# Kernel optimization log

Measured on AMD Instinct MI355X. Metric: run time of the kernel, lower is better.

The kernel has to match this reference:

```python
import jax, jax.numpy as jnp
import numpy as np

STEP_SIZE = 0.01  # init kwarg step_size

def _quad_grad(A, b, x):
    # grad of per-node quadratic: 2*A_n @ x_n + b_n ; shapes [N,D,D],[N,D],[N,D]
    return 2.0 * jnp.einsum('nij,nj->ni', A, x) + b

def setup_inputs() -> dict:
    key = jax.random.key(0)
    kA, kb, kx, ke = jax.random.split(key, 4)
    N, D, E = 20000, 64, 320000
    A = jax.random.normal(kA, (N, D, D), dtype=jnp.float32)
    b = jax.random.normal(kb, (N, D), dtype=jnp.float32)
    x = jax.random.normal(kx, (N, D), dtype=jnp.float32)
    edge_index = jax.random.randint(ke, (2, E), 0, N, dtype=jnp.int64)
    return {"A": A, "b": b, "x": x, "edge_index": edge_index, "num_layers": 10}

def reference(A, b, x, edge_index, num_layers):
    N, D = x.shape
    src, dst = edge_index[0], edge_index[1]
    # push-sum column-stochastic mixing weights: 1/out_degree incl. self-loop
    deg = jnp.ones((N,), x.dtype).at[src].add(1.0)
    inv_deg = (1.0 / deg)[:, None]  # [N,1]

    def mix(z):  # z: [N,F]
        msg = z[src] * inv_deg[src]  # gather + weight
        agg = jax.ops.segment_sum(msg, dst, num_segments=N)
        return agg + z * inv_deg  # self-loop term

    y = _quad_grad(A, b, x)
    u = x
    v = jnp.ones((N, 1), x.dtype)
    x0 = x
    x1 = x0
    for _ in range(num_layers):
        u = mix(u - STEP_SIZE * y)          # conv on u
        v = mix(v)                           # conv on v (push-sum weight)
        x1 = u * (1.0 / v)                   # inv_v * u
        g1 = _quad_grad(A, b, x1)
        g0 = _quad_grad(A, b, x0)
        y = mix(y) + g1 - g0                 # conv on y + gradient tracking
        x0 = x1
    comm_cost = jnp.asarray(3 * num_layers * src.shape[0], dtype=jnp.int64)
    return x1, comm_cost
```

## Files before the change

kernel.cpp:

```cpp
#include <hip/hip_runtime.h>
#include <hip/hip_bf16.h>
#include <hip/hip_fp16.h>

#define STEP 0.01f
#define D 64
#define NUM_LAYERS 10

union H4 { uint2 u; __half h[4]; };
union H8 { uint4 u; __half2 h2[4]; __half h[8]; };


__global__ void k_setup(float* __restrict__ degf, int* __restrict__ degd, int N) {
    int n = blockIdx.x * blockDim.x + threadIdx.x;
    if (n < N) { degf[n] = 1.0f; degd[n] = 0; }
}

__global__ void k_deg2(const int* __restrict__ ei, float* __restrict__ degf,
                       int* __restrict__ degd, int E) {
    int e = blockIdx.x * blockDim.x + threadIdx.x;
    if (e < E) {
        unsafeAtomicAdd(&degf[ei[e]], 1.0f);
        atomicAdd(&degd[ei[E + e]], 1);
    }
}

__global__ __launch_bounds__(1024) void k_scan(
        const int* __restrict__ degd, const float* __restrict__ degf,
        int* __restrict__ row_ptr, int* __restrict__ cursor,
        float* __restrict__ invdeg, int N, int E) {
    __shared__ int part[1024];
    int tid = threadIdx.x;
    int chunk = (N + 1023) / 1024;
    int lo = tid * chunk, hi = min(lo + chunk, N);
    int s = 0;
    for (int i = lo; i < hi; ++i) s += degd[i];
    part[tid] = s;
    __syncthreads();
    for (int off = 1; off < 1024; off <<= 1) {
        int v = (tid >= off) ? part[tid - off] : 0;
        __syncthreads();
        part[tid] += v;
        __syncthreads();
    }
    int base = (tid == 0) ? 0 : part[tid - 1];
    for (int i = lo; i < hi; ++i) {
        row_ptr[i] = base;
        cursor[i] = base;
        base += degd[i];
        invdeg[i] = 1.0f / degf[i];
    }
    if (tid == 1023) row_ptr[N] = E;
}

__global__ void k_scatter(const int* __restrict__ ei, int* __restrict__ cursor,
                          int* __restrict__ col, int E) {
    int e = blockIdx.x * blockDim.x + threadIdx.x;
    if (e < E) {
        int pos = atomicAdd(&cursor[ei[E + e]], 1);
        col[pos] = ei[e];
    }
}


__global__ __launch_bounds__(256) void k_init(
        const float* __restrict__ A, const float* __restrict__ b,
        const float* __restrict__ x, const float* __restrict__ invdeg,
        __half* __restrict__ Ah, __half2* __restrict__ msg,
        float* __restrict__ vw, float* __restrict__ x0, int N) {
    __shared__ __align__(16) float sx[D];
    __shared__ float syv[D];
    int n = blockIdx.x, t = threadIdx.x;
    int lane = t & 63, w = t >> 6, colgrp = lane & 15;
    if (t < D) sx[t] = x[(size_t)n * D + t];
    __syncthreads();
    const float* An = A + (size_t)n * D * D;
    __half* Ahn = Ah + (size_t)n * D * D;
    float4 xr = ((const float4*)sx)[colgrp];
    int rbase = w * 16 + (lane >> 4);
#pragma unroll
    for (int g = 0; g < 4; ++g) {
        int row = rbase + g * 4;
        float4 a = ((const float4*)(An + (size_t)row * D))[colgrp];
        H4 pk;
        pk.h[0] = __float2half(a.x);
        pk.h[1] = __float2half(a.y);
        pk.h[2] = __float2half(a.z);
        pk.h[3] = __float2half(a.w);
        ((uint2*)(Ahn + (size_t)row * D))[colgrp] = pk.u;
        float p = a.x * xr.x + a.y * xr.y + a.z * xr.z + a.w * xr.w;
        p += __shfl_xor(p, 1);
        p += __shfl_xor(p, 2);
        p += __shfl_xor(p, 4);
        p += __shfl_xor(p, 8);
        if (colgrp == 0) syv[row] = 2.0f * p + b[(size_t)n * D + row];
    }
    __syncthreads();
    if (t < D) {
        float wd = invdeg[n];
        float xv = sx[t];
        float yv = syv[t];
        msg[(size_t)n * D + t] = __floats2half2_rn((xv - STEP * yv) * wd, yv * wd);
        x0[(size_t)n * D + t] = xv;
        if (t == 0) vw[n] = wd;
    }
}


__global__ __launch_bounds__(256) void k_layer(
        const __half* __restrict__ Ah,
        const int* __restrict__ row_ptr, const int* __restrict__ col,
        const __half2* __restrict__ msg, const float* __restrict__ vw,
        const float* __restrict__ invdeg,
        __half2* __restrict__ msgn, float* __restrict__ vwn,
        float* __restrict__ x0, float* __restrict__ xout,
        int last_idx, float comm, int N) {
    int t = threadIdx.x;
    int lane = t & 63, w = t >> 6;
    int n = blockIdx.x * 4 + w;
    if (n >= N) return;

    int j = lane >> 4, q4 = lane & 15;
    int rs = row_ptr[n], re = row_ptr[n + 1];

    const uint4* Ap = (const uint4*)(Ah + (size_t)n * D * D);
    uint4 a[8];
#pragma unroll
    for (int k = 0; k < 8; ++k) a[k] = Ap[lane + 64 * k];

    size_t off = (size_t)n * D + lane;
    float2 msf = __half22float2(msg[off]);
    float x0v = x0[off];
    float vwn_self = vw[n];
    float invd = invdeg[n];

    float4 au = {0.f, 0.f, 0.f, 0.f}, ay = {0.f, 0.f, 0.f, 0.f};
    float av = 0.0f;
    for (int base = rs; base < re; base += 8) {
        int e0 = base + (j << 1), e1 = e0 + 1;
        bool b0 = e0 < re, b1 = e1 < re;
        int s0 = 0, s1 = 0;
        if (b0) s0 = col[e0];
        if (b1) s1 = col[e1];
        H8 m0, m1;
        m0.u = make_uint4(0u, 0u, 0u, 0u);
        m1.u = make_uint4(0u, 0u, 0u, 0u);
        float w0 = 0.f, w1 = 0.f;
        if (b0) m0.u = ((const uint4*)(msg + (size_t)s0 * D))[q4];
        if (b1) m1.u = ((const uint4*)(msg + (size_t)s1 * D))[q4];
        if (b0 && q4 == 0) w0 = vw[s0];
        if (b1 && q4 == 0) w1 = vw[s1];
        float2 f0 = __half22float2(m0.h2[0]);
        float2 f1 = __half22float2(m0.h2[1]);
        float2 f2 = __half22float2(m0.h2[2]);
        float2 f3 = __half22float2(m0.h2[3]);
        au.x += f0.x; ay.x += f0.y;
        au.y += f1.x; ay.y += f1.y;
        au.z += f2.x; ay.z += f2.y;
        au.w += f3.x; ay.w += f3.y;
        f0 = __half22float2(m1.h2[0]);
        f1 = __half22float2(m1.h2[1]);
        f2 = __half22float2(m1.h2[2]);
        f3 = __half22float2(m1.h2[3]);
        au.x += f0.x; ay.x += f0.y;
        au.y += f1.x; ay.y += f1.y;
        au.z += f2.x; ay.z += f2.y;
        au.w += f3.x; ay.w += f3.y;
        av += w0 + w1;
    }
    au.x += __shfl_xor(au.x, 16); au.y += __shfl_xor(au.y, 16);
    au.z += __shfl_xor(au.z, 16); au.w += __shfl_xor(au.w, 16);
    au.x += __shfl_xor(au.x, 32); au.y += __shfl_xor(au.y, 32);
    au.z += __shfl_xor(au.z, 32); au.w += __shfl_xor(au.w, 32);
    ay.x += __shfl_xor(ay.x, 16); ay.y += __shfl_xor(ay.y, 16);
    ay.z += __shfl_xor(ay.z, 16); ay.w += __shfl_xor(ay.w, 16);
    ay.x += __shfl_xor(ay.x, 32); ay.y += __shfl_xor(ay.y, 32);
    ay.z += __shfl_xor(ay.z, 32); ay.w += __shfl_xor(ay.w, 32);
    av += __shfl_xor(av, 16);
    av += __shfl_xor(av, 32);
    av = __shfl(av, 0);

    int src = lane >> 2, c = lane & 3;
    float ua = __shfl(au.x, src), ub = __shfl(au.y, src),
          uc = __shfl(au.z, src), ud = __shfl(au.w, src);
    float ya = __shfl(ay.x, src), yb = __shfl(ay.y, src),
          yc = __shfl(ay.z, src), yd = __shfl(ay.w, src);
    float ut = (c & 2) ? ((c & 1) ? ud : uc) : ((c & 1) ? ub : ua);
    float yt = (c & 2) ? ((c & 1) ? yd : yc) : ((c & 1) ? yb : ya);
    ut += msf.x;
    yt += msf.y;

    float vt = av + vwn_self;
    float rvt = __builtin_amdgcn_rcpf(vt);
    float x1 = ut * rvt;
    float dx = x1 - x0v;
    x0[off] = x1;
    if (xout) xout[off] = x1;
    if (lane == 0) vwn[n] = vt * invd;
    if (xout && n == 0 && lane == 0) xout[last_idx] = comm;

    int cb = (lane & 7) * 8;
    float dxv[8];
#pragma unroll
    for (int jj = 0; jj < 8; ++jj) dxv[jj] = __shfl(dx, cb + jj);

    float pk[8];
#pragma unroll
    for (int k = 0; k < 8; ++k) {
        H8 aa; aa.u = a[k];
        float p = 0.f;
#pragma unroll
        for (int jj = 0; jj < 8; ++jj)
            p += __half2float(aa.h[jj]) * dxv[jj];
        p += __shfl_xor(p, 1);
        p += __shfl_xor(p, 2);
        p += __shfl_xor(p, 4);
        pk[k] = p;
    }
    int srcg = (lane & 7) * 8;
    float pr[8];
#pragma unroll
    for (int k = 0; k < 8; ++k) pr[k] = __shfl(pk[k], srcg);
    int kk = lane >> 3;
    float prow = (kk & 4) ? ((kk & 2) ? ((kk & 1) ? pr[7] : pr[6])
                                      : ((kk & 1) ? pr[5] : pr[4]))
                          : ((kk & 2) ? ((kk & 1) ? pr[3] : pr[2])
                                      : ((kk & 1) ? pr[1] : pr[0]));
    float yn = yt + 2.0f * prow;
    msgn[off] = __floats2half2_rn((ut - STEP * yn) * invd, yn * invd);
}


extern "C" void kernel_launch(void* const* d_in, const int* in_sizes, int n_in,
                              void* d_out, int out_size, void* d_ws, size_t ws_size,
                              hipStream_t stream) {
    const float* A  = (const float*)d_in[0];
    const float* b  = (const float*)d_in[1];
    const float* x  = (const float*)d_in[2];
    const int*   ei = (const int*)d_in[3];

    const int N = in_sizes[1] / D;
    const int E = in_sizes[3] / 2;
    const size_t ND = (size_t)N * D;

    char* ws = (char*)d_ws;
    __half* Ah = (__half*)ws;
    __half2* msg0 = (__half2*)(ws + ND * D * sizeof(__half));
    __half2* msg1 = msg0 + ND;
    float* x0   = (float*)(msg1 + ND);
    float* vw0  = x0 + ND;
    float* vw1  = vw0 + N;
    float* invdeg = vw1 + N;
    float* degf = invdeg + N;
    int* degd    = (int*)(degf + N);
    int* row_ptr = degd + N;
    int* cursor  = row_ptr + N + 4;
    int* col     = cursor + N;

    k_setup<<<(N + 255) / 256, 256, 0, stream>>>(degf, degd, N);
    k_deg2<<<(E + 255) / 256, 256, 0, stream>>>(ei, degf, degd, E);
    k_scan<<<1, 1024, 0, stream>>>(degd, degf, row_ptr, cursor, invdeg, N, E);
    k_scatter<<<(E + 255) / 256, 256, 0, stream>>>(ei, cursor, col, E);
    k_init<<<N, 256, 0, stream>>>(A, b, x, invdeg, Ah, msg0, vw0, x0, N);

    float comm = (float)(3 * NUM_LAYERS * E);
    __half2 *mc = msg0, *mn = msg1;
    float *vc = vw0, *vn = vw1;
    for (int l = 0; l < NUM_LAYERS; ++l) {
        float* xout = (l == NUM_LAYERS - 1) ? (float*)d_out : nullptr;
        k_layer<<<(N + 3) / 4, 256, 0, stream>>>(Ah, row_ptr, col, mc, vc, invdeg,
                                                 mn, vn, x0, xout, out_size - 1, comm, N);
        __half2* tm = mc; mc = mn; mn = tm;
        float* tv = vc; vc = vn; vn = tv;
    }
}
```

Measured before the change: 960.6 us.

## Fuse init and all layers into one persistent cooperative kernel with grid syncs

Replaces the init kernel and ten per-layer launches with a single cooperative kernel of 1024 blocks. Each wave loops over nodes with a grid stride, and grid.sync separates the layers. The intent is to remove launch overhead and tail effects between layers. The cross-lane shuffle reductions are also replaced by per-wave shared-memory staging of dx and row results. The risk is grid-sync cost, lower occupancy from the fixed grid size, and bandwidth-bound layers that may gain little.

```diff
diff --git a/kernel.cpp b/kernel.cpp
--- a/kernel.cpp
+++ b/kernel.cpp
@@ -1,12 +1,14 @@
 #include <hip/hip_runtime.h>
-#include <hip/hip_bf16.h>
 #include <hip/hip_fp16.h>
+#include <hip/hip_cooperative_groups.h>
+
+namespace cg = cooperative_groups;
 
 #define STEP 0.01f
 #define D 64
 #define NUM_LAYERS 10
-
-union H4 { uint2 u; __half h[4]; };
+#define GRID 1024
+
 union H8 { uint4 u; __half2 h2[4]; __half h[8]; };
 
 
@@ -61,172 +63,179 @@
     }
 }
 
-
-__global__ __launch_bounds__(256) void k_init(
+__global__ void k_tail(float* __restrict__ out, int last_idx, int E) {
+    if (threadIdx.x == 0 && blockIdx.x == 0)
+        out[last_idx] = (float)(3 * NUM_LAYERS * E);
+}
+
+
+__global__ __launch_bounds__(256, 4) void k_fused(
         const float* __restrict__ A, const float* __restrict__ b,
-        const float* __restrict__ x, const float* __restrict__ invdeg,
-        __half* __restrict__ Ah, __half2* __restrict__ msg,
-        float* __restrict__ vw, float* __restrict__ x0, int N) {
-    __shared__ __align__(16) float sx[D];
-    __shared__ float syv[D];
-    int n = blockIdx.x, t = threadIdx.x;
-    int lane = t & 63, w = t >> 6, colgrp = lane & 15;
-    if (t < D) sx[t] = x[(size_t)n * D + t];
-    __syncthreads();
-    const float* An = A + (size_t)n * D * D;
-    __half* Ahn = Ah + (size_t)n * D * D;
-    float4 xr = ((const float4*)sx)[colgrp];
-    int rbase = w * 16 + (lane >> 4);
+        const float* __restrict__ x,
+        const int* __restrict__ row_ptr, const int* __restrict__ col,
+        const float* __restrict__ invdeg,
+        __half* __restrict__ Ah,
+        __half2* __restrict__ msg0, __half2* __restrict__ msg1,
+        float* __restrict__ vw0, float* __restrict__ vw1,
+        float* __restrict__ x0, float* __restrict__ xout,
+        int N) {
+    cg::grid_group gg = cg::this_grid();
+
+    __shared__ float sdx[4][D];
+    __shared__ float srow[4][D];
+    __shared__ float4 sg[4][2][16];
+
+    int t = threadIdx.x, lane = t & 63, w = t >> 6;
+    int wid = blockIdx.x * 4 + w;
+    int nw = GRID * 4;
+    int kq = lane >> 3;
+    int cb = (lane & 7) * 8;
+    int j = lane >> 4, q4 = lane & 15;
+
+    for (int n = wid; n < N; n += nw) {
+        size_t off = (size_t)n * D + lane;
+        float xv = x[off];
+        sdx[w][lane] = xv;
+        const float4* An = (const float4*)(A + (size_t)n * D * D);
+        uint4* Ahn = (uint4*)(Ah + (size_t)n * D * D);
 #pragma unroll
-    for (int g = 0; g < 4; ++g) {
-        int row = rbase + g * 4;
-        float4 a = ((const float4*)(An + (size_t)row * D))[colgrp];
-        H4 pk;
-        pk.h[0] = __float2half(a.x);
-        pk.h[1] = __float2half(a.y);
-        pk.h[2] = __float2half(a.z);
-        pk.h[3] = __float2half(a.w);
-        ((uint2*)(Ahn + (size_t)row * D))[colgrp] = pk.u;
-        float p = a.x * xr.x + a.y * xr.y + a.z * xr.z + a.w * xr.w;
-        p += __shfl_xor(p, 1);
-        p += __shfl_xor(p, 2);
-        p += __shfl_xor(p, 4);
-        p += __shfl_xor(p, 8);
-        if (colgrp == 0) syv[row] = 2.0f * p + b[(size_t)n * D + row];
-    }
-    __syncthreads();
-    if (t < D) {
+        for (int k = 0; k < 8; ++k) {
+            int row = kq + 8 * k;
+            int fidx = row * (D / 4) + (cb >> 2);
+            float4 f0 = An[fidx];
+            float4 f1 = An[fidx + 1];
+            H8 pk;
+            pk.h[0] = __float2half(f0.x);
+            pk.h[1] = __float2half(f0.y);
+            pk.h[2] = __float2half(f0.z);
+            pk.h[3] = __float2half(f0.w);
+            pk.h[4] = __float2half(f1.x);
+            pk.h[5] = __float2half(f1.y);
+            pk.h[6] = __float2half(f1.z);
+            pk.h[7] = __float2half(f1.w);
+            Ahn[lane + 64 * k] = pk.u;
+            float p = f0.x * sdx[w][cb + 0] + f0.y * sdx[w][cb + 1]
+                    + f0.z * sdx[w][cb + 2] + f0.w * sdx[w][cb + 3]
+                    + f1.x * sdx[w][cb + 4] + f1.y * sdx[w][cb + 5]
+                    + f1.z * sdx[w][cb + 6] + f1.w * sdx[w][cb + 7];
+            p += __shfl_xor(p, 1);
+            p += __shfl_xor(p, 2);
+            p += __shfl_xor(p, 4);
+            if ((lane & 7) == 0) srow[w][row] = p;
+        }
+        float yv = 2.0f * srow[w][lane] + b[off];
         float wd = invdeg[n];
-        float xv = sx[t];
-        float yv = syv[t];
-        msg[(size_t)n * D + t] = __floats2half2_rn((xv - STEP * yv) * wd, yv * wd);
-        x0[(size_t)n * D + t] = xv;
-        if (t == 0) vw[n] = wd;
-    }
-}
-
-
-__global__ __launch_bounds__(256) void k_layer(
-        const __half* __restrict__ Ah,
-        const int* __restrict__ row_ptr, const int* __restrict__ col,
-        const __half2* __restrict__ msg, const float* __restrict__ vw,
-        const float* __restrict__ invdeg,
-        __half2* __restrict__ msgn, float* __restrict__ vwn,
-        float* __restrict__ x0, float* __restrict__ xout,
-        int last_idx, float comm, int N) {
-    int t = threadIdx.x;
-    int lane = t & 63, w = t >> 6;
-    int n = blockIdx.x * 4 + w;
-    if (n >= N) return;
-
-    int j = lane >> 4, q4 = lane & 15;
-    int rs = row_ptr[n], re = row_ptr[n + 1];
-
-    const uint4* Ap = (const uint4*)(Ah + (size_t)n * D * D);
-    uint4 a[8];
+        msg0[off] = __floats2half2_rn((xv - STEP * yv) * wd, yv * wd);
+        x0[off] = xv;
+        if (lane == 0) vw0[n] = wd;
+    }
+    __threadfence();
+    gg.sync();
+
+    for (int l = 0; l < NUM_LAYERS; ++l) {
+        const __half2* mc = (l & 1) ? msg1 : msg0;
+        __half2* mn = (l & 1) ? msg0 : msg1;
+        const float* vc = (l & 1) ? vw1 : vw0;
+        float* vn = (l & 1) ? vw0 : vw1;
+        float* xo = (l == NUM_LAYERS - 1) ? xout : nullptr;
+
+        for (int n = wid; n < N; n += nw) {
+            int rs = row_ptr[n], re = row_ptr[n + 1];
+
+            const uint4* Ap = (const uint4*)(Ah + (size_t)n * D * D);
+            uint4 a[8];
 #pragma unroll
-    for (int k = 0; k < 8; ++k) a[k] = Ap[lane + 64 * k];
-
-    size_t off = (size_t)n * D + lane;
-    float2 msf = __half22float2(msg[off]);
-    float x0v = x0[off];
-    float vwn_self = vw[n];
-    float invd = invdeg[n];
-
-    float4 au = {0.f, 0.f, 0.f, 0.f}, ay = {0.f, 0.f, 0.f, 0.f};
-    float av = 0.0f;
-    for (int base = rs; base < re; base += 8) {
-        int e0 = base + (j << 1), e1 = e0 + 1;
-        bool b0 = e0 < re, b1 = e1 < re;
-        int s0 = 0, s1 = 0;
-        if (b0) s0 = col[e0];
-        if (b1) s1 = col[e1];
-        H8 m0, m1;
-        m0.u = make_uint4(0u, 0u, 0u, 0u);
-        m1.u = make_uint4(0u, 0u, 0u, 0u);
-        float w0 = 0.f, w1 = 0.f;
-        if (b0) m0.u = ((const uint4*)(msg + (size_t)s0 * D))[q4];
-        if (b1) m1.u = ((const uint4*)(msg + (size_t)s1 * D))[q4];
-        if (b0 && q4 == 0) w0 = vw[s0];
-        if (b1 && q4 == 0) w1 = vw[s1];
-        float2 f0 = __half22float2(m0.h2[0]);
-        float2 f1 = __half22float2(m0.h2[1]);
-        float2 f2 = __half22float2(m0.h2[2]);
-        float2 f3 = __half22float2(m0.h2[3]);
-        au.x += f0.x; ay.x += f0.y;
-        au.y += f1.x; ay.y += f1.y;
-        au.z += f2.x; ay.z += f2.y;
-        au.w += f3.x; ay.w += f3.y;
-        f0 = __half22float2(m1.h2[0]);
-        f1 = __half22float2(m1.h2[1]);
-        f2 = __half22float2(m1.h2[2]);
-        f3 = __half22float2(m1.h2[3]);
-        au.x += f0.x; ay.x += f0.y;
-        au.y += f1.x; ay.y += f1.y;
-        au.z += f2.x; ay.z += f2.y;
-        au.w += f3.x; ay.w += f3.y;
-        av += w0 + w1;
-    }
-    au.x += __shfl_xor(au.x, 16); au.y += __shfl_xor(au.y, 16);
-    au.z += __shfl_xor(au.z, 16); au.w += __shfl_xor(au.w, 16);
-    au.x += __shfl_xor(au.x, 32); au.y += __shfl_xor(au.y, 32);
-    au.z += __shfl_xor(au.z, 32); au.w += __shfl_xor(au.w, 32);
-    ay.x += __shfl_xor(ay.x, 16); ay.y += __shfl_xor(ay.y, 16);
-    ay.z += __shfl_xor(ay.z, 16); ay.w += __shfl_xor(ay.w, 16);
-    ay.x += __shfl_xor(ay.x, 32); ay.y += __shfl_xor(ay.y, 32);
-    ay.z += __shfl_xor(ay.z, 32); ay.w += __shfl_xor(ay.w, 32);
-    av += __shfl_xor(av, 16);
-    av += __shfl_xor(av, 32);
-    av = __shfl(av, 0);
-
-    int src = lane >> 2, c = lane & 3;
-    float ua = __shfl(au.x, src), ub = __shfl(au.y, src),
-          uc = __shfl(au.z, src), ud = __shfl(au.w, src);
-    float ya = __shfl(ay.x, src), yb = __shfl(ay.y, src),
-          yc = __shfl(ay.z, src), yd = __shfl(ay.w, src);
-    float ut = (c & 2) ? ((c & 1) ? ud : uc) : ((c & 1) ? ub : ua);
-    float yt = (c & 2) ? ((c & 1) ? yd : yc) : ((c & 1) ? yb : ya);
-    ut += msf.x;
-    yt += msf.y;
-
-    float vt = av + vwn_self;
-    float rvt = __builtin_amdgcn_rcpf(vt);
-    float x1 = ut * rvt;
-    float dx = x1 - x0v;
-    x0[off] = x1;
-    if (xout) xout[off] = x1;
-    if (lane == 0) vwn[n] = vt * invd;
-    if (xout && n == 0 && lane == 0) xout[last_idx] = comm;
-
-    int cb = (lane & 7) * 8;
-    float dxv[8];
+            for (int k = 0; k < 8; ++k) a[k] = Ap[lane + 64 * k];
+
+            size_t off = (size_t)n * D + lane;
+            float2 msf = __half22float2(mc[off]);
+            float x0v = x0[off];
+            float vws = vc[n];
+            float invd = invdeg[n];
+
+            float4 au = {0.f, 0.f, 0.f, 0.f}, ay = {0.f, 0.f, 0.f, 0.f};
+            float av = 0.0f;
+            for (int base = rs; base < re; base += 8) {
+                int e0 = base + (j << 1), e1 = e0 + 1;
+                bool b0 = e0 < re, b1 = e1 < re;
+                int s0 = 0, s1 = 0;
+                if (b0) s0 = col[e0];
+                if (b1) s1 = col[e1];
+                H8 m0, m1;
+                m0.u = make_uint4(0u, 0u, 0u, 0u);
+                m1.u = make_uint4(0u, 0u, 0u, 0u);
+                float w0 = 0.f, w1 = 0.f;
+                if (b0) m0.u = ((const uint4*)(mc + (size_t)s0 * D))[q4];
+                if (b1) m1.u = ((const uint4*)(mc + (size_t)s1 * D))[q4];
+                if (b0 && q4 == 0) w0 = vc[s0];
+                if (b1 && q4 == 0) w1 = vc[s1];
+                float2 f0 = __half22float2(m0.h2[0]);
+                float2 f1 = __half22float2(m0.h2[1]);
+                float2 f2 = __half22float2(m0.h2[2]);
+                float2 f3 = __half22float2(m0.h2[3]);
+                au.x += f0.x; ay.x += f0.y;
+                au.y += f1.x; ay.y += f1.y;
+                au.z += f2.x; ay.z += f2.y;
+                au.w += f3.x; ay.w += f3.y;
+                f0 = __half22float2(m1.h2[0]);
+                f1 = __half22float2(m1.h2[1]);
+                f2 = __half22float2(m1.h2[2]);
+                f3 = __half22float2(m1.h2[3]);
+                au.x += f0.x; ay.x += f0.y;
+                au.y += f1.x; ay.y += f1.y;
+                au.z += f2.x; ay.z += f2.y;
+                au.w += f3.x; ay.w += f3.y;
+                av += w0 + w1;
+            }
+            au.x += __shfl_xor(au.x, 16); au.y += __shfl_xor(au.y, 16);
+            au.z += __shfl_xor(au.z, 16); au.w += __shfl_xor(au.w, 16);
+            au.x += __shfl_xor(au.x, 32); au.y += __shfl_xor(au.y, 32);
+            au.z += __shfl_xor(au.z, 32); au.w += __shfl_xor(au.w, 32);
+            ay.x += __shfl_xor(ay.x, 16); ay.y += __shfl_xor(ay.y, 16);
+            ay.z += __shfl_xor(ay.z, 16); ay.w += __shfl_xor(ay.w, 16);
+            ay.x += __shfl_xor(ay.x, 32); ay.y += __shfl_xor(ay.y, 32);
+            ay.z += __shfl_xor(ay.z, 32); ay.w += __shfl_xor(ay.w, 32);
+            av += __shfl_xor(av, 16);
+            av += __shfl_xor(av, 32);
+            av = __shfl(av, 0);
+
+            if (j == 0) { sg[w][0][q4] = au; sg[w][1][q4] = ay; }
+            float ut = ((const float*)sg[w][0])[lane] + msf.x;
+            float yt = ((const float*)sg[w][1])[lane] + msf.y;
+
+            float vt = av + vws;
+            float rvt = __builtin_amdgcn_rcpf(vt);
+            float x1 = ut * rvt;
+            float dx = x1 - x0v;
+            x0[off] = x1;
+            if (xo) xo[off] = x1;
+            if (lane == 0) vn[n] = vt * invd;
+
+            sdx[w][lane] = dx;
 #pragma unroll
-    for (int jj = 0; jj < 8; ++jj) dxv[jj] = __shfl(dx, cb + jj);
-
-    float pk[8];
-#pragma unroll
-    for (int k = 0; k < 8; ++k) {
-        H8 aa; aa.u = a[k];
-        float p = 0.f;
-#pragma unroll
-        for (int jj = 0; jj < 8; ++jj)
-            p += __half2float(aa.h[jj]) * dxv[jj];
-        p += __shfl_xor(p, 1);
-        p += __shfl_xor(p, 2);
-        p += __shfl_xor(p, 4);
-        pk[k] = p;
-    }
-    int srcg = (lane & 7) * 8;
-    float pr[8];
-#pragma unroll
-    for (int k = 0; k < 8; ++k) pr[k] = __shfl(pk[k], srcg);
-    int kk = lane >> 3;
-    float prow = (kk & 4) ? ((kk & 2) ? ((kk & 1) ? pr[7] : pr[6])
-                                      : ((kk & 1) ? pr[5] : pr[4]))
-                          : ((kk & 2) ? ((kk & 1) ? pr[3] : pr[2])
-                                      : ((kk & 1) ? pr[1] : pr[0]));
-    float yn = yt + 2.0f * prow;
-    msgn[off] = __floats2half2_rn((ut - STEP * yn) * invd, yn * invd);
+            for (int k = 0; k < 8; ++k) {
+                H8 aa; aa.u = a[k];
+                float p = __half2float(aa.h[0]) * sdx[w][cb + 0]
+                        + __half2float(aa.h[1]) * sdx[w][cb + 1]
+                        + __half2float(aa.h[2]) * sdx[w][cb + 2]
+                        + __half2float(aa.h[3]) * sdx[w][cb + 3]
+                        + __half2float(aa.h[4]) * sdx[w][cb + 4]
+                        + __half2float(aa.h[5]) * sdx[w][cb + 5]
+                        + __half2float(aa.h[6]) * sdx[w][cb + 6]
+                        + __half2float(aa.h[7]) * sdx[w][cb + 7];
+                p += __shfl_xor(p, 1);
+                p += __shfl_xor(p, 2);
+                p += __shfl_xor(p, 4);
+                if ((lane & 7) == 0) srow[w][kq + 8 * k] = p;
+            }
+            float yn = yt + 2.0f * srow[w][lane];
+            mn[off] = __floats2half2_rn((ut - STEP * yn) * invd, yn * invd);
+        }
+        if (l != NUM_LAYERS - 1) {
+            __threadfence();
+            gg.sync();
+        }
+    }
 }
 
 
@@ -260,16 +269,19 @@
     k_deg2<<<(E + 255) / 256, 256, 0, stream>>>(ei, degf, degd, E);
     k_scan<<<1, 1024, 0, stream>>>(degd, degf, row_ptr, cursor, invdeg, N, E);
     k_scatter<<<(E + 255) / 256, 256, 0, stream>>>(ei, cursor, col, E);
-    k_init<<<N, 256, 0, stream>>>(A, b, x, invdeg, Ah, msg0, vw0, x0, N);
-
-    float comm = (float)(3 * NUM_LAYERS * E);
-    __half2 *mc = msg0, *mn = msg1;
-    float *vc = vw0, *vn = vw1;
-    for (int l = 0; l < NUM_LAYERS; ++l) {
-        float* xout = (l == NUM_LAYERS - 1) ? (float*)d_out : nullptr;
-        k_layer<<<(N + 3) / 4, 256, 0, stream>>>(Ah, row_ptr, col, mc, vc, invdeg,
-                                                 mn, vn, x0, xout, out_size - 1, comm, N);
-        __half2* tm = mc; mc = mn; mn = tm;
-        float* tv = vc; vc = vn; vn = tv;
-    }
-}
+
+    float* xout = (float*)d_out;
+    int Nv = N;
+
+    void* args[] = {
+        (void*)&A, (void*)&b, (void*)&x,
+        (void*)&row_ptr, (void*)&col, (void*)&invdeg,
+        (void*)&Ah, (void*)&msg0, (void*)&msg1,
+        (void*)&vw0, (void*)&vw1, (void*)&x0, (void*)&xout,
+        (void*)&Nv
+    };
+    hipLaunchCooperativeKernel((void*)k_fused, dim3(GRID), dim3(256),
+                               args, 0, stream);
+
+    k_tail<<<1, 64, 0, stream>>>(xout, out_size - 1, E);
+}
```

Measured after the change: 3.295 ms. +243.0%, slower.

## Split fused layer kernel into separate gather and matvec kernels

Applied to the files above, without the earlier changes.

Splits each layer into a neighbor-gather kernel, which writes dx, u and y to global scratch buffers, and a separate kernel that loads the fp16 A block and computes the matvec. Each kernel then holds fewer live registers, since the gather no longer keeps the 8 uint4 A fragments resident, and each should get higher occupancy. The cost is an extra round trip of three N*D float buffers through memory and double the number of launches per layer. The comm-cost write moves to a small tail kernel.

```diff
diff --git a/kernel.cpp b/kernel.cpp
--- a/kernel.cpp
+++ b/kernel.cpp
@@ -61,6 +61,11 @@
     }
 }
 
+__global__ void k_tail(float* __restrict__ out, int last_idx, int E) {
+    if (threadIdx.x == 0 && blockIdx.x == 0)
+        out[last_idx] = (float)(3 * NUM_LAYERS * E);
+}
+
 
 __global__ __launch_bounds__(256) void k_init(
         const float* __restrict__ A, const float* __restrict__ b,
@@ -106,14 +111,13 @@
 }
 
 
-__global__ __launch_bounds__(256) void k_layer(
-        const __half* __restrict__ Ah,
+__global__ __launch_bounds__(256) void k_gather(
         const int* __restrict__ row_ptr, const int* __restrict__ col,
         const __half2* __restrict__ msg, const float* __restrict__ vw,
         const float* __restrict__ invdeg,
-        __half2* __restrict__ msgn, float* __restrict__ vwn,
-        float* __restrict__ x0, float* __restrict__ xout,
-        int last_idx, float comm, int N) {
+        float* __restrict__ vwn, float* __restrict__ x0, float* __restrict__ xout,
+        float* __restrict__ dxb, float* __restrict__ utb, float* __restrict__ ytb,
+        int N) {
     int t = threadIdx.x;
     int lane = t & 63, w = t >> 6;
     int n = blockIdx.x * 4 + w;
@@ -121,17 +125,6 @@
 
     int j = lane >> 4, q4 = lane & 15;
     int rs = row_ptr[n], re = row_ptr[n + 1];
-
-    const uint4* Ap = (const uint4*)(Ah + (size_t)n * D * D);
-    uint4 a[8];
-#pragma unroll
-    for (int k = 0; k < 8; ++k) a[k] = Ap[lane + 64 * k];
-
-    size_t off = (size_t)n * D + lane;
-    float2 msf = __half22float2(msg[off]);
-    float x0v = x0[off];
-    float vwn_self = vw[n];
-    float invd = invdeg[n];
 
     float4 au = {0.f, 0.f, 0.f, 0.f}, ay = {0.f, 0.f, 0.f, 0.f};
     float av = 0.0f;
@@ -167,6 +160,13 @@
         au.w += f3.x; ay.w += f3.y;
         av += w0 + w1;
     }
+
+    size_t off = (size_t)n * D + lane;
+    float2 msf = __half22float2(msg[off]);
+    float x0v = x0[off];
+    float vws = vw[n];
+    float invd = invdeg[n];
+
     au.x += __shfl_xor(au.x, 16); au.y += __shfl_xor(au.y, 16);
     au.z += __shfl_xor(au.z, 16); au.w += __shfl_xor(au.w, 16);
     au.x += __shfl_xor(au.x, 32); au.y += __shfl_xor(au.y, 32);
@@ -189,19 +189,46 @@
     ut += msf.x;
     yt += msf.y;
 
-    float vt = av + vwn_self;
+    float vt = av + vws;
     float rvt = __builtin_amdgcn_rcpf(vt);
     float x1 = ut * rvt;
     float dx = x1 - x0v;
     x0[off] = x1;
     if (xout) xout[off] = x1;
     if (lane == 0) vwn[n] = vt * invd;
-    if (xout && n == 0 && lane == 0) xout[last_idx] = comm;
-
+
+    dxb[off] = dx;
+    utb[off] = ut;
+    ytb[off] = yt;
+}
+
+
+__global__ __launch_bounds__(256) void k_matvec(
+        const __half* __restrict__ Ah,
+        const float* __restrict__ dxb, const float* __restrict__ utb,
+        const float* __restrict__ ytb, const float* __restrict__ invdeg,
+        __half2* __restrict__ msgn, int N) {
+    int t = threadIdx.x;
+    int lane = t & 63, w = t >> 6;
+    int n = blockIdx.x * 4 + w;
+    if (n >= N) return;
+
+    size_t off = (size_t)n * D + lane;
     int cb = (lane & 7) * 8;
-    float dxv[8];
-#pragma unroll
-    for (int jj = 0; jj < 8; ++jj) dxv[jj] = __shfl(dx, cb + jj);
+
+    float ut = utb[off];
+    float yt = ytb[off];
+    float invd = invdeg[n];
+    const float4* dxp = (const float4*)(dxb + (size_t)n * D);
+    float4 d0 = dxp[cb >> 2];
+    float4 d1 = dxp[(cb >> 2) + 1];
+
+    const uint4* Ap = (const uint4*)(Ah + (size_t)n * D * D);
+    uint4 a[8];
+#pragma unroll
+    for (int k = 0; k < 8; ++k) a[k] = Ap[lane + 64 * k];
+
+    float dxv[8] = {d0.x, d0.y, d0.z, d0.w, d1.x, d1.y, d1.z, d1.w};
 
     float pk[8];
 #pragma unroll
@@ -255,6 +282,9 @@
     int* row_ptr = degd + N;
     int* cursor  = row_ptr + N + 4;
     int* col     = cursor + N;
+    float* dxb  = (float*)(col + E);
+    float* utb  = dxb + ND;
+    float* ytb  = utb + ND;
 
     k_setup<<<(N + 255) / 256, 256, 0, stream>>>(degf, degd, N);
     k_deg2<<<(E + 255) / 256, 256, 0, stream>>>(ei, degf, degd, E);
@@ -262,14 +292,17 @@
     k_scatter<<<(E + 255) / 256, 256, 0, stream>>>(ei, cursor, col, E);
     k_init<<<N, 256, 0, stream>>>(A, b, x, invdeg, Ah, msg0, vw0, x0, N);
 
-    float comm = (float)(3 * NUM_LAYERS * E);
     __half2 *mc = msg0, *mn = msg1;
     float *vc = vw0, *vn = vw1;
+    int nb = (N + 3) / 4;
     for (int l = 0; l < NUM_LAYERS; ++l) {
         float* xout = (l == NUM_LAYERS - 1) ? (float*)d_out : nullptr;
-        k_layer<<<(N + 3) / 4, 256, 0, stream>>>(Ah, row_ptr, col, mc, vc, invdeg,
-                                                 mn, vn, x0, xout, out_size - 1, comm, N);
+        k_gather<<<nb, 256, 0, stream>>>(row_ptr, col, mc, vc, invdeg,
+                                         vn, x0, xout, dxb, utb, ytb, N);
+        k_matvec<<<nb, 256, 0, stream>>>(Ah, dxb, utb, ytb, invdeg, mn, N);
         __half2* tm = mc; mc = mn; mn = tm;
         float* tv = vc; vc = vn; vn = tv;
     }
-}
+
+    k_tail<<<1, 64, 0, stream>>>((float*)d_out, out_size - 1, E);
+}
```

Result: slower. 1.028 ms (+7.0%).
